# Performance work log

Measured on AMD Instinct MI355X. Metric: run time of the kernel, lower is better.

The kernel has to match this reference:

```python
import jax, jax.numpy as jnp
import numpy as np

B, T, N, F_IN, F_OUT, H = 32, 32, 256, 32, 32, 256
NEG_SLOPE = 0.2  # GATConv default leaky-relu slope


def setup_inputs() -> dict:
    key = jax.random.key(0)
    ks = jax.random.split(key, 12)
    x = jax.random.normal(ks[0], (B, T, N, F_IN), dtype=jnp.float32)
    u = jax.random.uniform(ks[1], (B, T, N, N))
    w = jax.random.uniform(ks[2], (B, T, N, N))
    adj = jnp.where(u < 0.1, w, 0.0).astype(jnp.float32)
    # GAT params (heads=1, concat=False)
    W = jax.random.normal(ks[3], (F_IN, F_OUT), dtype=jnp.float32) / np.sqrt(F_IN)
    a_src = jax.random.normal(ks[4], (F_OUT,), dtype=jnp.float32) / np.sqrt(F_OUT)
    a_dst = jax.random.normal(ks[5], (F_OUT,), dtype=jnp.float32) / np.sqrt(F_OUT)
    gat_b = jnp.zeros((F_OUT,), dtype=jnp.float32)
    # LSTM params (PyTorch layout, gate order i,f,g,o)
    IN = N * F_OUT
    s = 1.0 / np.sqrt(H)
    W_ih = jax.random.uniform(ks[6], (4 * H, IN), minval=-s, maxval=s, dtype=jnp.float32)
    W_hh = jax.random.uniform(ks[7], (4 * H, H), minval=-s, maxval=s, dtype=jnp.float32)
    b_ih = jax.random.uniform(ks[8], (4 * H,), minval=-s, maxval=s, dtype=jnp.float32)
    b_hh = jax.random.uniform(ks[9], (4 * H,), minval=-s, maxval=s, dtype=jnp.float32)
    # output Linear
    Wo = jax.random.uniform(ks[10], (N, H), minval=-s, maxval=s, dtype=jnp.float32)
    bo = jax.random.uniform(ks[11], (N,), minval=-s, maxval=s, dtype=jnp.float32)
    return {"x": x, "adj": adj, "W": W, "a_src": a_src, "a_dst": a_dst,
            "gat_b": gat_b, "W_ih": W_ih, "W_hh": W_hh, "b_ih": b_ih,
            "b_hh": b_hh, "Wo": Wo, "bo": bo}


def _gat(x, adj, W, a_src, a_dst, gat_b):
    # batched over (B,T). h: [B,T,N,F_OUT]
    h = jnp.einsum('btnf,fo->btno', x, W)
    s_src = jnp.einsum('btno,o->btn', h, a_src)  # contribution of source node j
    s_dst = jnp.einsum('btno,o->btn', h, a_dst)  # contribution of target node i
    # e[i,j] = LeakyReLU(a_dst.h_i + a_src.h_j)
    e = jax.nn.leaky_relu(s_dst[..., :, None] + s_src[..., None, :], NEG_SLOPE)
    # edge (row=j -> col=i) exists iff adj[j,i] != 0; GATConv adds self-loops
    mask = (jnp.swapaxes(adj, -1, -2) != 0) | jnp.eye(N, dtype=bool)
    alpha = jax.nn.softmax(jnp.where(mask, e, -jnp.inf), axis=-1)  # softmax over sources j per target i
    return jnp.einsum('btij,btjo->btio', alpha, h) + gat_b


def _lstm_last(seq, W_ih, W_hh, b_ih, b_hh):
    # seq: [B,T,IN] -> last hidden state [B,H]
    def step(carry, x_t):
        h_prev, c_prev = carry
        gates = x_t @ W_ih.T + h_prev @ W_hh.T + (b_ih + b_hh)
        i, f, g, o = jnp.split(gates, 4, axis=-1)
        c = jax.nn.sigmoid(f) * c_prev + jax.nn.sigmoid(i) * jnp.tanh(g)
        h = jax.nn.sigmoid(o) * jnp.tanh(c)
        return (h, c), None
    init = (jnp.zeros((seq.shape[0], H), seq.dtype), jnp.zeros((seq.shape[0], H), seq.dtype))
    (h_last, _), _ = jax.lax.scan(step, init, jnp.swapaxes(seq, 0, 1))
    return h_last


def reference(x, adj, W, a_src, a_dst, gat_b, W_ih, W_hh, b_ih, b_hh, Wo, bo):
    gat_out = _gat(x, adj, W, a_src, a_dst, gat_b)            # [B,T,N,F_OUT]
    seq = gat_out.reshape(gat_out.shape[0], gat_out.shape[1], -1)  # [B,T,N*F_OUT]
    h_last = _lstm_last(seq, W_ih, W_hh, b_ih, b_hh)          # [B,H]
    return h_last @ Wo.T + bo                                  # [B,N]
```

## Files before the change

kernel.cpp:

```cpp
#include <hip/hip_runtime.h>
#include <cstdint>

constexpr int B_ = 32, T_ = 32, N_ = 256, FIN = 32, FOUT = 32, H_ = 256;
constexpr int IN_ = N_ * FOUT;
constexpr int G4  = 4 * H_;
constexpr int BT  = B_ * T_;
#define NEG_SLOPE 0.2f

typedef _Float16 half8 __attribute__((ext_vector_type(8)));
typedef _Float16 h2    __attribute__((ext_vector_type(2)));
typedef float    f4    __attribute__((ext_vector_type(4)));

__device__ inline uint32_t pkh2(float a, float b) {
    union { uint32_t u; _Float16 h[2]; } z;
    z.h[0] = (_Float16)a; z.h[1] = (_Float16)b; return z.u;
}
__device__ inline float f16lo(uint32_t u){ union{uint32_t u; _Float16 h[2];} z; z.u=u; return (float)z.h[0]; }
__device__ inline float f16hi(uint32_t u){ union{uint32_t u; _Float16 h[2];} z; z.u=u; return (float)z.h[1]; }

__device__ inline float dot2f(uint32_t w, uint32_t h, float acc) {
    union { uint32_t u; h2 v; } a, b; a.u = w; b.u = h;
#if __has_builtin(__builtin_amdgcn_fdot2)
    return __builtin_amdgcn_fdot2(a.v, b.v, acc, false);
#else
    return acc + (float)a.v.x * (float)b.v.x + (float)a.v.y * (float)b.v.y;
#endif
}

__device__ inline void gload16(const void* g, void* l) {
    __builtin_amdgcn_global_load_lds(
        (const __attribute__((address_space(1))) void*)g,
        (__attribute__((address_space(3))) void*)l, 16, 0, 0);
}

__global__ __launch_bounds__(256) void gat_kernel(
    const float* __restrict__ x, const float* __restrict__ adj,
    const float* __restrict__ W, const float* __restrict__ a_src,
    const float* __restrict__ a_dst, const float* __restrict__ gat_b,
    _Float16* __restrict__ seq_hi, _Float16* __restrict__ seq_lo)
{
    const int bt = blockIdx.x;
    const int i  = threadIdx.x;
    __shared__ float Ws[FIN * FOUT];
    __shared__ float hs[N_ * 36];
    __shared__ float ssrc[N_];
    __shared__ float asv[FOUT], adv[FOUT], gbv[FOUT];

    for (int t = i; t < FIN * FOUT; t += 256) Ws[t] = W[t];
    if (i < FOUT) { asv[i] = a_src[i]; adv[i] = a_dst[i]; gbv[i] = gat_b[i]; }

    float xr[FIN];
    const float* xrow = x + ((size_t)bt * N_ + i) * FIN;
    #pragma unroll
    for (int f4i = 0; f4i < FIN / 4; ++f4i) {
        float4 v = reinterpret_cast<const float4*>(xrow)[f4i];
        xr[4*f4i] = v.x; xr[4*f4i+1] = v.y; xr[4*f4i+2] = v.z; xr[4*f4i+3] = v.w;
    }
    __syncthreads();

    float hr[FOUT];
    #pragma unroll
    for (int k4 = 0; k4 < FOUT / 4; ++k4) {
        float ax = 0.f, ay = 0.f, az = 0.f, aw = 0.f;
        #pragma unroll
        for (int f = 0; f < FIN; ++f) {
            float4 w4 = *reinterpret_cast<const float4*>(&Ws[f*FOUT + 4*k4]);
            ax += xr[f]*w4.x; ay += xr[f]*w4.y; az += xr[f]*w4.z; aw += xr[f]*w4.w;
        }
        hr[4*k4] = ax; hr[4*k4+1] = ay; hr[4*k4+2] = az; hr[4*k4+3] = aw;
    }
    float ss = 0.f, sd = 0.f;
    #pragma unroll
    for (int k = 0; k < FOUT; ++k) { ss += hr[k]*asv[k]; sd += hr[k]*adv[k]; }
    #pragma unroll
    for (int k = 0; k < FOUT; ++k) hs[i*36 + k] = hr[k];
    ssrc[i] = ss;
    __syncthreads();

    float acc[FOUT];
    #pragma unroll
    for (int k = 0; k < FOUT; ++k) acc[k] = 0.f;
    float l = 0.f;
    const float* adjcol = adj + (size_t)bt * N_ * N_ + i;
    #pragma unroll 4
    for (int j = 0; j < N_; ++j) {
        float a = adjcol[(size_t)j * N_];
        float e = sd + ssrc[j];
        e = e > 0.f ? e : NEG_SLOPE * e;
        float p = ((a != 0.f) || (j == i)) ? __expf(e) : 0.f;
        l += p;
        #pragma unroll
        for (int k4 = 0; k4 < FOUT/4; ++k4) {
            float4 h4 = *reinterpret_cast<const float4*>(&hs[j*36 + 4*k4]);
            acc[4*k4]   += p * h4.x;
            acc[4*k4+1] += p * h4.y;
            acc[4*k4+2] += p * h4.z;
            acc[4*k4+3] += p * h4.w;
        }
    }
    float inv = 1.f / l;
    _Float16 vhi[FOUT], vlo[FOUT];
    #pragma unroll
    for (int k = 0; k < FOUT; ++k) {
        float v = acc[k]*inv + gbv[k];
        _Float16 h = (_Float16)v;
        vhi[k] = h;
        vlo[k] = (_Float16)(v - (float)h);
    }
    _Float16* ohi = seq_hi + (size_t)bt * IN_ + i * FOUT;
    _Float16* olo = seq_lo + (size_t)bt * IN_ + i * FOUT;
    #pragma unroll
    for (int k8 = 0; k8 < FOUT/8; ++k8) {
        *reinterpret_cast<half8*>(ohi + 8*k8) = *reinterpret_cast<half8*>(&vhi[8*k8]);
        *reinterpret_cast<half8*>(olo + 8*k8) = *reinterpret_cast<half8*>(&vlo[8*k8]);
    }
}

__global__ __launch_bounds__(256) void pack_wih_kernel(
    const float* __restrict__ Wih, _Float16* __restrict__ out)
{
    int idx = (blockIdx.x * 256 + threadIdx.x) * 8;
    float4 v0 = *reinterpret_cast<const float4*>(Wih + idx);
    float4 v1 = *reinterpret_cast<const float4*>(Wih + idx + 4);
    half8 o;
    o[0]=(_Float16)v0.x; o[1]=(_Float16)v0.y; o[2]=(_Float16)v0.z; o[3]=(_Float16)v0.w;
    o[4]=(_Float16)v1.x; o[5]=(_Float16)v1.y; o[6]=(_Float16)v1.z; o[7]=(_Float16)v1.w;
    *reinterpret_cast<half8*>(out + idx) = o;
}

__global__ __launch_bounds__(256) void pack_whh_kernel(
    const float* __restrict__ Whh, uint32_t* __restrict__ pwv, uint32_t* __restrict__ pws)
{
    int g = blockIdx.x * 256 + threadIdx.x;
    const float* row = Whh + (size_t)g * H_;
    #pragma unroll
    for (int p = 0; p < 128; ++p) {
        float2 v = *reinterpret_cast<const float2*>(row + 2*p);
        uint32_t u = pkh2(v.x, v.y);
        if (p < 100) pwv[p * 1024 + g] = u;
        else { int pp = p - 100; pws[(pp >> 2) * 4096 + g * 4 + (pp & 3)] = u; }
    }
}

__global__ __launch_bounds__(256, 4) void gemm_kernel(
    const _Float16* __restrict__ Ahi, const _Float16* __restrict__ Alo,
    const _Float16* __restrict__ Bh, float* __restrict__ G)
{
    __shared__ __align__(16) _Float16 As[128 * 32];
    __shared__ __align__(16) _Float16 Bs[128 * 32];
    const int t = threadIdx.x;
    const int L = t & 63, w = t >> 6;
    const int wm = w & 1, wn = w >> 1;
    const int m0 = blockIdx.y * 128, n0 = blockIdx.x * 128;
    const int kz = blockIdx.z * 1024;

    f4 acc[4][4] = {};
    const int q0 = t, q1 = t + 256;
    const int row0 = q0 >> 2, kc0 = q0 & 3;
    const int row1 = q1 >> 2, kc1 = q1 & 3;
    const int la = (L & 15) * 32 + (L >> 4) * 8;

    #pragma unroll
    for (int pass = 0; pass < 2; ++pass) {
        const _Float16* Ab = pass ? Alo : Ahi;
        const _Float16* A0 = Ab + (size_t)(m0 + row0) * IN_ + kz + kc0 * 8;
        const _Float16* A1 = Ab + (size_t)(m0 + row1) * IN_ + kz + kc1 * 8;
        const _Float16* B0 = Bh + (size_t)(n0 + row0) * IN_ + kz + kc0 * 8;
        const _Float16* B1 = Bh + (size_t)(n0 + row1) * IN_ + kz + kc1 * 8;
        for (int kb = 0; kb < 1024; kb += 32) {
            __syncthreads();
            gload16(A0 + kb, &As[q0 * 8]);
            gload16(A1 + kb, &As[q1 * 8]);
            gload16(B0 + kb, &Bs[q0 * 8]);
            gload16(B1 + kb, &Bs[q1 * 8]);
            __syncthreads();
            half8 af[4], bf[4];
            #pragma unroll
            for (int mi = 0; mi < 4; ++mi)
                af[mi] = *reinterpret_cast<const half8*>(&As[(wm*64 + mi*16) * 32 + la]);
            #pragma unroll
            for (int ni = 0; ni < 4; ++ni)
                bf[ni] = *reinterpret_cast<const half8*>(&Bs[(wn*64 + ni*16) * 32 + la]);
            #pragma unroll
            for (int mi = 0; mi < 4; ++mi)
                #pragma unroll
                for (int ni = 0; ni < 4; ++ni)
                    acc[mi][ni] = __builtin_amdgcn_mfma_f32_16x16x32_f16(
                        af[mi], bf[ni], acc[mi][ni], 0, 0, 0);
        }
    }
    const int cn = n0 + wn * 64 + (L & 15);
    const int rm = m0 + wm * 64 + (L >> 4) * 4;
    #pragma unroll
    for (int mi = 0; mi < 4; ++mi)
        #pragma unroll
        for (int ni = 0; ni < 4; ++ni)
            #pragma unroll
            for (int r = 0; r < 4; ++r)
                atomicAdd(&G[(size_t)(rm + mi*16 + r) * G4 + cn + ni*16], acc[mi][ni][r]);
}

__global__ __launch_bounds__(1024, 4) void lstm_kernel(
    const float* __restrict__ G, const uint32_t* __restrict__ pwv,
    const uint32_t* __restrict__ pws,
    const float* __restrict__ b_ih, const float* __restrict__ b_hh,
    const float* __restrict__ Wo, const float* __restrict__ bo,
    float* __restrict__ out)
{
    const int b = blockIdx.x;
    const int g = threadIdx.x;
    __shared__ __align__(16) uint32_t hsp[128];
    __shared__ float gsh[G4];
    __shared__ __align__(16) uint32_t wl[3 * 4096];

    uint32_t wv[88];
    #pragma unroll
    for (int p = 0; p < 88; ++p) wv[p] = pwv[p * 1024 + g];
    #pragma unroll
    for (int p = 88; p < 100; ++p) {
        int pp = p - 88;
        wl[(pp >> 2) * 4096 + g * 4 + (pp & 3)] = pwv[p * 1024 + g];
    }
    if (g < 128) hsp[g] = 0u;
    float c = 0.f;
    const float bias = b_ih[g] + b_hh[g];
    const float* Gb = G + (size_t)b * T_ * G4 + g;
    const uint4* pws4 = reinterpret_cast<const uint4*>(pws);
    const uint4* wl4  = reinterpret_cast<const uint4*>(wl);
    const uint4* hsp4 = reinterpret_cast<const uint4*>(hsp);
    __syncthreads();

    for (int t = 0; t < T_; ++t) {
        float acc = bias + Gb[(size_t)t * G4];
        #pragma unroll
        for (int q = 0; q < 32; ++q) {
            uint4 h4 = hsp4[q];
            uint4 w4;
            if (q < 22) {
                w4.x = wv[4*q]; w4.y = wv[4*q+1]; w4.z = wv[4*q+2]; w4.w = wv[4*q+3];
            } else if (q < 25) {
                w4 = wl4[(q - 22) * 1024 + g];
            } else {
                w4 = pws4[(q - 25) * 1024 + g];
            }
            acc = dot2f(w4.x, h4.x, acc);
            acc = dot2f(w4.y, h4.y, acc);
            acc = dot2f(w4.z, h4.z, acc);
            acc = dot2f(w4.w, h4.w, acc);
        }
        gsh[g] = acc;
        __syncthreads();
        if (g < H_) {
            float xi = gsh[g], xf = gsh[H_ + g], xg = gsh[2*H_ + g], xo = gsh[3*H_ + g];
            float si = 1.f / (1.f + __expf(-xi));
            float sf = 1.f / (1.f + __expf(-xf));
            float so = 1.f / (1.f + __expf(-xo));
            float eg = __expf(2.f * xg);
            float tg = 1.f - 2.f / (eg + 1.f);
            c = sf * c + si * tg;
            float ec = __expf(2.f * c);
            float th = 1.f - 2.f / (ec + 1.f);
            reinterpret_cast<_Float16*>(hsp)[g] = (_Float16)(so * th);
        }
        __syncthreads();
    }
    if (g < N_) {
        const float* worow = Wo + (size_t)g * H_;
        float o = bo[g];
        #pragma unroll
        for (int q = 0; q < 32; ++q) {
            uint4 hq = hsp4[q];
            float4 w0 = *reinterpret_cast<const float4*>(worow + q*8);
            float4 w1 = *reinterpret_cast<const float4*>(worow + q*8 + 4);
            o += w0.x * f16lo(hq.x) + w0.y * f16hi(hq.x)
               + w0.z * f16lo(hq.y) + w0.w * f16hi(hq.y)
               + w1.x * f16lo(hq.z) + w1.y * f16hi(hq.z)
               + w1.z * f16lo(hq.w) + w1.w * f16hi(hq.w);
        }
        out[(size_t)b * N_ + g] = o;
    }
}

extern "C" void kernel_launch(void* const* d_in, const int* in_sizes, int n_in,
                              void* d_out, int out_size, void* d_ws, size_t ws_size,
                              hipStream_t stream) {
    const float* x     = (const float*)d_in[0];
    const float* adj   = (const float*)d_in[1];
    const float* W     = (const float*)d_in[2];
    const float* a_src = (const float*)d_in[3];
    const float* a_dst = (const float*)d_in[4];
    const float* gat_b = (const float*)d_in[5];
    const float* W_ih  = (const float*)d_in[6];
    const float* W_hh  = (const float*)d_in[7];
    const float* b_ih  = (const float*)d_in[8];
    const float* b_hh  = (const float*)d_in[9];
    const float* Wo    = (const float*)d_in[10];
    const float* bo    = (const float*)d_in[11];
    float* out = (float*)d_out;

    _Float16* seq_hi = (_Float16*)d_ws;
    _Float16* seq_lo = seq_hi + (size_t)BT * IN_;
    _Float16* wih_h  = seq_lo + (size_t)BT * IN_;
    float*    G      = (float*)(wih_h + (size_t)G4 * IN_);
    uint32_t* pwv    = (uint32_t*)(G + (size_t)BT * G4);
    uint32_t* pws    = pwv + 100 * 1024;

    hipMemsetAsync(G, 0, (size_t)BT * G4 * sizeof(float), stream);
    pack_whh_kernel<<<dim3(4), dim3(256), 0, stream>>>(W_hh, pwv, pws);
    pack_wih_kernel<<<dim3(4096), dim3(256), 0, stream>>>(W_ih, wih_h);
    gat_kernel<<<dim3(BT), dim3(256), 0, stream>>>(x, adj, W, a_src, a_dst, gat_b, seq_hi, seq_lo);
    gemm_kernel<<<dim3(8, 8, 8), dim3(256), 0, stream>>>(seq_hi, seq_lo, wih_h, G);
    lstm_kernel<<<dim3(B_), dim3(1024), 0, stream>>>(G, pwv, pws, b_ih, b_hh, Wo, bo, out);
}
```

Baseline: 645.7 us.

## Drop hi/lo fp16 split of GAT output, use fp16 dot2 aggregation

The GAT output is now written as a single fp16 array instead of a hi/lo pair. This halves the GEMM's A-matrix traffic and removes its second K pass. The GAT aggregation stores h as fp16 pairs interleaved by node and accumulates with packed dot2 instructions. The LSTM splits its recurrent weights differently across registers, LDS (six chunks, bulk-copied as uint4) and global memory, and prefetches the next timestep's input gate value. These changes trade accuracy (fp16 activations and attention weights) for lower memory traffic and fewer GEMM passes, with some risk of exceeding tolerance.

```diff
diff --git a/kernel.cpp b/kernel.cpp
--- a/kernel.cpp
+++ b/kernel.cpp
@@ -37,12 +37,12 @@
     const float* __restrict__ x, const float* __restrict__ adj,
     const float* __restrict__ W, const float* __restrict__ a_src,
     const float* __restrict__ a_dst, const float* __restrict__ gat_b,
-    _Float16* __restrict__ seq_hi, _Float16* __restrict__ seq_lo)
+    _Float16* __restrict__ seq)
 {
     const int bt = blockIdx.x;
     const int i  = threadIdx.x;
     __shared__ float Ws[FIN * FOUT];
-    __shared__ float hs[N_ * 36];
+    __shared__ __align__(16) uint32_t hpp[128 * 36];
     __shared__ float ssrc[N_];
     __shared__ float asv[FOUT], adv[FOUT], gbv[FOUT];
 
@@ -72,8 +72,10 @@
     float ss = 0.f, sd = 0.f;
     #pragma unroll
     for (int k = 0; k < FOUT; ++k) { ss += hr[k]*asv[k]; sd += hr[k]*adv[k]; }
-    #pragma unroll
-    for (int k = 0; k < FOUT; ++k) hs[i*36 + k] = hr[k];
+    _Float16* hp16 = reinterpret_cast<_Float16*>(hpp);
+    #pragma unroll
+    for (int k = 0; k < FOUT; ++k)
+        hp16[(i >> 1) * 72 + 2*k + (i & 1)] = (_Float16)hr[k];
     ssrc[i] = ss;
     __syncthreads();
 
@@ -82,38 +84,36 @@
     for (int k = 0; k < FOUT; ++k) acc[k] = 0.f;
     float l = 0.f;
     const float* adjcol = adj + (size_t)bt * N_ * N_ + i;
-    #pragma unroll 4
-    for (int j = 0; j < N_; ++j) {
-        float a = adjcol[(size_t)j * N_];
-        float e = sd + ssrc[j];
-        e = e > 0.f ? e : NEG_SLOPE * e;
-        float p = ((a != 0.f) || (j == i)) ? __expf(e) : 0.f;
-        l += p;
-        #pragma unroll
-        for (int k4 = 0; k4 < FOUT/4; ++k4) {
-            float4 h4 = *reinterpret_cast<const float4*>(&hs[j*36 + 4*k4]);
-            acc[4*k4]   += p * h4.x;
-            acc[4*k4+1] += p * h4.y;
-            acc[4*k4+2] += p * h4.z;
-            acc[4*k4+3] += p * h4.w;
+    #pragma unroll 2
+    for (int q = 0; q < 128; ++q) {
+        const int j0 = 2*q, j1 = 2*q + 1;
+        float a0 = adjcol[(size_t)j0 * N_];
+        float a1 = adjcol[(size_t)j1 * N_];
+        float e0 = sd + ssrc[j0]; e0 = e0 > 0.f ? e0 : NEG_SLOPE * e0;
+        float e1 = sd + ssrc[j1]; e1 = e1 > 0.f ? e1 : NEG_SLOPE * e1;
+        float p0 = ((a0 != 0.f) || (j0 == i)) ? __expf(e0) : 0.f;
+        float p1 = ((a1 != 0.f) || (j1 == i)) ? __expf(e1) : 0.f;
+        l += p0 + p1;
+        uint32_t pk = pkh2(p0, p1);
+        const uint32_t* hq = &hpp[q * 36];
+        #pragma unroll
+        for (int k4 = 0; k4 < 8; ++k4) {
+            uint4 hv = *reinterpret_cast<const uint4*>(&hq[4*k4]);
+            acc[4*k4+0] = dot2f(pk, hv.x, acc[4*k4+0]);
+            acc[4*k4+1] = dot2f(pk, hv.y, acc[4*k4+1]);
+            acc[4*k4+2] = dot2f(pk, hv.z, acc[4*k4+2]);
+            acc[4*k4+3] = dot2f(pk, hv.w, acc[4*k4+3]);
         }
     }
     float inv = 1.f / l;
-    _Float16 vhi[FOUT], vlo[FOUT];
-    #pragma unroll
-    for (int k = 0; k < FOUT; ++k) {
-        float v = acc[k]*inv + gbv[k];
-        _Float16 h = (_Float16)v;
-        vhi[k] = h;
-        vlo[k] = (_Float16)(v - (float)h);
-    }
-    _Float16* ohi = seq_hi + (size_t)bt * IN_ + i * FOUT;
-    _Float16* olo = seq_lo + (size_t)bt * IN_ + i * FOUT;
-    #pragma unroll
-    for (int k8 = 0; k8 < FOUT/8; ++k8) {
-        *reinterpret_cast<half8*>(ohi + 8*k8) = *reinterpret_cast<half8*>(&vhi[8*k8]);
-        *reinterpret_cast<half8*>(olo + 8*k8) = *reinterpret_cast<half8*>(&vlo[8*k8]);
-    }
+    _Float16 vh[FOUT];
+    #pragma unroll
+    for (int k = 0; k < FOUT; ++k)
+        vh[k] = (_Float16)(acc[k]*inv + gbv[k]);
+    _Float16* orow = seq + (size_t)bt * IN_ + i * FOUT;
+    #pragma unroll
+    for (int k8 = 0; k8 < FOUT/8; ++k8)
+        *reinterpret_cast<half8*>(orow + 8*k8) = *reinterpret_cast<half8*>(&vh[8*k8]);
 }
 
 __global__ __launch_bounds__(256) void pack_wih_kernel(
@@ -129,7 +129,8 @@
 }
 
 __global__ __launch_bounds__(256) void pack_whh_kernel(
-    const float* __restrict__ Whh, uint32_t* __restrict__ pwv, uint32_t* __restrict__ pws)
+    const float* __restrict__ Whh, uint32_t* __restrict__ pwv,
+    uint32_t* __restrict__ pwl, uint32_t* __restrict__ pws)
 {
     int g = blockIdx.x * 256 + threadIdx.x;
     const float* row = Whh + (size_t)g * H_;
@@ -137,14 +138,15 @@
     for (int p = 0; p < 128; ++p) {
         float2 v = *reinterpret_cast<const float2*>(row + 2*p);
         uint32_t u = pkh2(v.x, v.y);
-        if (p < 100) pwv[p * 1024 + g] = u;
-        else { int pp = p - 100; pws[(pp >> 2) * 4096 + g * 4 + (pp & 3)] = u; }
+        if (p < 64) pwv[p * 1024 + g] = u;
+        else if (p < 88) { int pp = p - 64; pwl[(pp >> 2) * 4096 + g * 4 + (pp & 3)] = u; }
+        else            { int pp = p - 88; pws[(pp >> 2) * 4096 + g * 4 + (pp & 3)] = u; }
     }
 }
 
 __global__ __launch_bounds__(256, 4) void gemm_kernel(
-    const _Float16* __restrict__ Ahi, const _Float16* __restrict__ Alo,
-    const _Float16* __restrict__ Bh, float* __restrict__ G)
+    const _Float16* __restrict__ A, const _Float16* __restrict__ Bh,
+    float* __restrict__ G)
 {
     __shared__ __align__(16) _Float16 As[128 * 32];
     __shared__ __align__(16) _Float16 Bs[128 * 32];
@@ -160,34 +162,30 @@
     const int row1 = q1 >> 2, kc1 = q1 & 3;
     const int la = (L & 15) * 32 + (L >> 4) * 8;
 
-    #pragma unroll
-    for (int pass = 0; pass < 2; ++pass) {
-        const _Float16* Ab = pass ? Alo : Ahi;
-        const _Float16* A0 = Ab + (size_t)(m0 + row0) * IN_ + kz + kc0 * 8;
-        const _Float16* A1 = Ab + (size_t)(m0 + row1) * IN_ + kz + kc1 * 8;
-        const _Float16* B0 = Bh + (size_t)(n0 + row0) * IN_ + kz + kc0 * 8;
-        const _Float16* B1 = Bh + (size_t)(n0 + row1) * IN_ + kz + kc1 * 8;
-        for (int kb = 0; kb < 1024; kb += 32) {
-            __syncthreads();
-            gload16(A0 + kb, &As[q0 * 8]);
-            gload16(A1 + kb, &As[q1 * 8]);
-            gload16(B0 + kb, &Bs[q0 * 8]);
-            gload16(B1 + kb, &Bs[q1 * 8]);
-            __syncthreads();
-            half8 af[4], bf[4];
-            #pragma unroll
-            for (int mi = 0; mi < 4; ++mi)
-                af[mi] = *reinterpret_cast<const half8*>(&As[(wm*64 + mi*16) * 32 + la]);
+    const _Float16* A0 = A + (size_t)(m0 + row0) * IN_ + kz + kc0 * 8;
+    const _Float16* A1 = A + (size_t)(m0 + row1) * IN_ + kz + kc1 * 8;
+    const _Float16* B0 = Bh + (size_t)(n0 + row0) * IN_ + kz + kc0 * 8;
+    const _Float16* B1 = Bh + (size_t)(n0 + row1) * IN_ + kz + kc1 * 8;
+    for (int kb = 0; kb < 1024; kb += 32) {
+        __syncthreads();
+        gload16(A0 + kb, &As[q0 * 8]);
+        gload16(A1 + kb, &As[q1 * 8]);
+        gload16(B0 + kb, &Bs[q0 * 8]);
+        gload16(B1 + kb, &Bs[q1 * 8]);
+        __syncthreads();
+        half8 af[4], bf[4];
+        #pragma unroll
+        for (int mi = 0; mi < 4; ++mi)
+            af[mi] = *reinterpret_cast<const half8*>(&As[(wm*64 + mi*16) * 32 + la]);
+        #pragma unroll
+        for (int ni = 0; ni < 4; ++ni)
+            bf[ni] = *reinterpret_cast<const half8*>(&Bs[(wn*64 + ni*16) * 32 + la]);
+        #pragma unroll
+        for (int mi = 0; mi < 4; ++mi)
             #pragma unroll
             for (int ni = 0; ni < 4; ++ni)
-                bf[ni] = *reinterpret_cast<const half8*>(&Bs[(wn*64 + ni*16) * 32 + la]);
-            #pragma unroll
-            for (int mi = 0; mi < 4; ++mi)
-                #pragma unroll
-                for (int ni = 0; ni < 4; ++ni)
-                    acc[mi][ni] = __builtin_amdgcn_mfma_f32_16x16x32_f16(
-                        af[mi], bf[ni], acc[mi][ni], 0, 0, 0);
-        }
+                acc[mi][ni] = __builtin_amdgcn_mfma_f32_16x16x32_f16(
+                    af[mi], bf[ni], acc[mi][ni], 0, 0, 0);
     }
     const int cn = n0 + wn * 64 + (L & 15);
     const int rm = m0 + wm * 64 + (L >> 4) * 4;
@@ -200,9 +198,9 @@
                 atomicAdd(&G[(size_t)(rm + mi*16 + r) * G4 + cn + ni*16], acc[mi][ni][r]);
 }
 
-__global__ __launch_bounds__(1024, 4) void lstm_kernel(
+__global__ __launch_bounds__(1024) void lstm_kernel(
     const float* __restrict__ G, const uint32_t* __restrict__ pwv,
-    const uint32_t* __restrict__ pws,
+    const uint32_t* __restrict__ pwl, const uint32_t* __restrict__ pws,
     const float* __restrict__ b_ih, const float* __restrict__ b_hh,
     const float* __restrict__ Wo, const float* __restrict__ bo,
     float* __restrict__ out)
@@ -211,15 +209,16 @@
     const int g = threadIdx.x;
     __shared__ __align__(16) uint32_t hsp[128];
     __shared__ float gsh[G4];
-    __shared__ __align__(16) uint32_t wl[3 * 4096];
-
-    uint32_t wv[88];
-    #pragma unroll
-    for (int p = 0; p < 88; ++p) wv[p] = pwv[p * 1024 + g];
-    #pragma unroll
-    for (int p = 88; p < 100; ++p) {
-        int pp = p - 88;
-        wl[(pp >> 2) * 4096 + g * 4 + (pp & 3)] = pwv[p * 1024 + g];
+    __shared__ __align__(16) uint32_t wl[6 * 4096];
+
+    uint32_t wv[64];
+    #pragma unroll
+    for (int p = 0; p < 64; ++p) wv[p] = pwv[p * 1024 + g];
+    {
+        const uint4* s = reinterpret_cast<const uint4*>(pwl);
+        uint4* d = reinterpret_cast<uint4*>(wl);
+        #pragma unroll
+        for (int r = 0; r < 6; ++r) d[r * 1024 + g] = s[r * 1024 + g];
     }
     if (g < 128) hsp[g] = 0u;
     float c = 0.f;
@@ -228,20 +227,22 @@
     const uint4* pws4 = reinterpret_cast<const uint4*>(pws);
     const uint4* wl4  = reinterpret_cast<const uint4*>(wl);
     const uint4* hsp4 = reinterpret_cast<const uint4*>(hsp);
+    float gnext = Gb[0];
     __syncthreads();
 
     for (int t = 0; t < T_; ++t) {
-        float acc = bias + Gb[(size_t)t * G4];
+        float acc = bias + gnext;
+        if (t + 1 < T_) gnext = Gb[(size_t)(t + 1) * G4];
         #pragma unroll
         for (int q = 0; q < 32; ++q) {
             uint4 h4 = hsp4[q];
             uint4 w4;
-            if (q < 22) {
+            if (q < 16) {
                 w4.x = wv[4*q]; w4.y = wv[4*q+1]; w4.z = wv[4*q+2]; w4.w = wv[4*q+3];
-            } else if (q < 25) {
-                w4 = wl4[(q - 22) * 1024 + g];
+            } else if (q < 22) {
+                w4 = wl4[(q - 16) * 1024 + g];
             } else {
-                w4 = pws4[(q - 25) * 1024 + g];
+                w4 = pws4[(q - 22) * 1024 + g];
             }
             acc = dot2f(w4.x, h4.x, acc);
             acc = dot2f(w4.y, h4.y, acc);
@@ -298,17 +299,17 @@
     const float* bo    = (const float*)d_in[11];
     float* out = (float*)d_out;
 
-    _Float16* seq_hi = (_Float16*)d_ws;
-    _Float16* seq_lo = seq_hi + (size_t)BT * IN_;
-    _Float16* wih_h  = seq_lo + (size_t)BT * IN_;
-    float*    G      = (float*)(wih_h + (size_t)G4 * IN_);
-    uint32_t* pwv    = (uint32_t*)(G + (size_t)BT * G4);
-    uint32_t* pws    = pwv + 100 * 1024;
+    _Float16* seq   = (_Float16*)d_ws;
+    _Float16* wih_h = seq + (size_t)BT * IN_;
+    float*    G     = (float*)(wih_h + (size_t)G4 * IN_);
+    uint32_t* pwv   = (uint32_t*)(G + (size_t)BT * G4);
+    uint32_t* pwl   = pwv + 64 * 1024;
+    uint32_t* pws   = pwl + 24 * 1024;
 
     hipMemsetAsync(G, 0, (size_t)BT * G4 * sizeof(float), stream);
-    pack_whh_kernel<<<dim3(4), dim3(256), 0, stream>>>(W_hh, pwv, pws);
+    pack_whh_kernel<<<dim3(4), dim3(256), 0, stream>>>(W_hh, pwv, pwl, pws);
     pack_wih_kernel<<<dim3(4096), dim3(256), 0, stream>>>(W_ih, wih_h);
-    gat_kernel<<<dim3(BT), dim3(256), 0, stream>>>(x, adj, W, a_src, a_dst, gat_b, seq_hi, seq_lo);
-    gemm_kernel<<<dim3(8, 8, 8), dim3(256), 0, stream>>>(seq_hi, seq_lo, wih_h, G);
-    lstm_kernel<<<dim3(B_), dim3(1024), 0, stream>>>(G, pwv, pws, b_ih, b_hh, Wo, bo, out);
-}
+    gat_kernel<<<dim3(BT), dim3(256), 0, stream>>>(x, adj, W, a_src, a_dst, gat_b, seq);
+    gemm_kernel<<<dim3(8, 8, 8), dim3(256), 0, stream>>>(seq, wih_h, G);
+    lstm_kernel<<<dim3(B_), dim3(1024), 0, stream>>>(G, pwv, pwl, pws, b_ih, b_hh, Wo, bo, out);
+}
```

Result: faster. 612.3 us (-5.2%).
